# Kernel tuning notes

Measured on AMD Instinct MI355X. Metric: run time of the kernel, lower is better.

The kernel has to match this reference:

```python
import jax, jax.numpy as jnp
import numpy as np

I, H = 1, 16  # input_size, hidden_size


def setup_inputs() -> dict:
    key = jax.random.key(0)
    ks = jax.random.split(key, 7)
    B, T = 8192, 512
    s_ih = 1.0 / np.sqrt(H)
    return {
        "x": jax.random.normal(ks[0], (B, T, I), dtype=jnp.float32),
        "W_ih": jax.random.uniform(ks[1], (3 * H, I), minval=-s_ih, maxval=s_ih, dtype=jnp.float32),
        "W_hh": jax.random.uniform(ks[2], (3 * H, H), minval=-s_ih, maxval=s_ih, dtype=jnp.float32),
        "b_ih": jax.random.uniform(ks[3], (3 * H,), minval=-s_ih, maxval=s_ih, dtype=jnp.float32),
        "b_hh": jax.random.uniform(ks[4], (3 * H,), minval=-s_ih, maxval=s_ih, dtype=jnp.float32),
        "fc_w": jax.random.uniform(ks[5], (1, H), minval=-s_ih, maxval=s_ih, dtype=jnp.float32),
        "fc_b": jax.random.uniform(ks[6], (1,), minval=-s_ih, maxval=s_ih, dtype=jnp.float32),
    }


def _gru_last_hidden(x, W_ih, W_hh, b_ih, b_hh):
    # Precompute input projections for all timesteps: [B, T, 3H]
    xp = jnp.einsum("bti,gi->btg", x, W_ih) + b_ih
    xp = jnp.transpose(xp, (1, 0, 2))  # [T, B, 3H] for scan over time
    B = x.shape[0]
    h0 = jnp.zeros((B, H), dtype=x.dtype)

    def step(h, xt):
        # PyTorch GRU gate equations (gate order: r, z, n)
        gh = h @ W_hh.T + b_hh  # [B, 3H]
        xr, xz, xn = xt[:, :H], xt[:, H:2 * H], xt[:, 2 * H:]
        hr, hz, hn = gh[:, :H], gh[:, H:2 * H], gh[:, 2 * H:]
        r = jax.nn.sigmoid(xr + hr)
        z = jax.nn.sigmoid(xz + hz)
        n = jnp.tanh(xn + r * hn)
        h_new = (1.0 - z) * n + z * h
        return h_new, None

    h_last, _ = jax.lax.scan(step, h0, xp)
    return h_last  # [B, H]


def reference(x, W_ih, W_hh, b_ih, b_hh, fc_w, fc_b):
    # Dropout is identity in eval mode
    h_last = _gru_last_hidden(x, W_ih, W_hh, b_ih, b_hh)
    return h_last @ fc_w.T + fc_b  # [B, 1]
```

## Files before the change

### kernel.cpp

```cpp
#include <hip/hip_runtime.h>

namespace {

constexpr int T_LEN = 512;
constexpr float LOG2E = 1.4426950408889634f;

typedef _Float16 half4 __attribute__((ext_vector_type(4)));
typedef _Float16 half2v __attribute__((ext_vector_type(2)));
typedef float v4f __attribute__((ext_vector_type(4)));

__device__ __forceinline__ float fexp2(float a) {
#if __has_builtin(__builtin_amdgcn_exp2f)
    return __builtin_amdgcn_exp2f(a);
#else
    return exp2f(a);
#endif
}

__device__ __forceinline__ v4f mfma16h(half4 a, half4 b, v4f c) {
#if __has_builtin(__builtin_amdgcn_mfma_f32_16x16x16f16)
    return __builtin_amdgcn_mfma_f32_16x16x16f16(a, b, c, 0, 0, 0);
#else
    v4f d;
    asm volatile("v_mfma_f32_16x16x16_f16 %0, %1, %2, %3\n\ts_nop 7\n\ts_nop 7"
                 : "=v"(d) : "v"(a), "v"(b), "v"(c));
    return d;
#endif
}

__device__ __forceinline__ unsigned pk_f16(float a, float b) {
#if __has_builtin(__builtin_amdgcn_cvt_pkrtz)
    return __builtin_bit_cast(unsigned, __builtin_amdgcn_cvt_pkrtz(a, b));
#else
    half2v r; r[0] = (_Float16)a; r[1] = (_Float16)b;
    return __builtin_bit_cast(unsigned, r);
#endif
}

template<int OFF>
__device__ __forceinline__ unsigned ds_swz_u(unsigned v) {
    return (unsigned)__builtin_amdgcn_ds_swizzle((int)v, OFF);
}

__device__ __forceinline__ float gru_pair(float drp, float dzp, float dnp,
                                          float xt, float wihn, float bihn,
                                          float hp) {
    float Er = fexp2(drp);
    float Ez = fexp2(dzp);
    float pr = 1.0f + Er;
    float pz = 1.0f + Ez;
    float ip = __builtin_amdgcn_rcpf(pr * pz);
    float r  = ip * pz;
    float z  = ip * pr;
    float xn = __builtin_fmaf(xt, wihn, bihn);
    float v  = __builtin_fmaf(r, dnp, xn);
    float n  = __builtin_fmaf(-2.0f, __builtin_amdgcn_rcpf(1.0f + fexp2(v)), 1.0f);
    return __builtin_fmaf(z, hp - n, n);
}

__global__ __launch_bounds__(64) void gru_mfma8(
        const float* __restrict__ x,
        const float* __restrict__ W_ih,
        const float* __restrict__ W_hh,
        const float* __restrict__ b_ih,
        const float* __restrict__ b_hh,
        const float* __restrict__ fc_w,
        const float* __restrict__ fc_b,
        float* __restrict__ out) {
    const int L  = threadIdx.x;
    const int e  = L & 15;
    const int g  = L >> 4;
    const int jD = g * 4;
    const int ehi  = (e >> 3) & 1;
    const int ecol = e & 7;
    const int be   = blockIdx.x * 8 + ecol;
    const int r0   = jD + 2 * ehi;

    const float sR = -LOG2E;
    const float sN = 2.0f * LOG2E;

    half4 ar_hi, ar_lo, az_hi, az_lo, an_hi, an_lo;
#pragma unroll
    for (int i = 0; i < 4; ++i) {
        float wr = W_hh[(0  + e) * 16 + jD + i] * sR;
        float wz = W_hh[(16 + e) * 16 + jD + i] * sR;
        float wn = W_hh[(32 + e) * 16 + jD + i] * sN;
        _Float16 rh = (_Float16)wr; ar_hi[i] = rh; ar_lo[i] = (_Float16)(wr - (float)rh);
        _Float16 zh = (_Float16)wz; az_hi[i] = zh; az_lo[i] = (_Float16)(wz - (float)zh);
        _Float16 nh = (_Float16)wn; an_hi[i] = nh; an_lo[i] = (_Float16)(wn - (float)nh);
    }

    float wihr[4], wihz[4], biasr[4], biasz[4];
    v4f cn_const;
#pragma unroll
    for (int i = 0; i < 4; ++i) {
        int rj = jD + i;
        wihr[i]  = W_ih[rj]      * sR;
        wihz[i]  = W_ih[16 + rj] * sR;
        biasr[i] = (b_ih[rj]      + b_hh[rj])      * sR;
        biasz[i] = (b_ih[16 + rj] + b_hh[16 + rj]) * sR;
        cn_const[i] = b_hh[32 + rj] * sN;
    }
    const float wihn0 = W_ih[32 + r0]     * sN;
    const float wihn1 = W_ih[32 + r0 + 1] * sN;
    const float bihn0 = b_ih[32 + r0]     * sN;
    const float bihn1 = b_ih[32 + r0 + 1] * sN;

    const float4* xb = (const float4*)(x + (size_t)be * T_LEN);
    float4 xc0 = xb[0], xc1 = xb[1], xc2 = xb[2], xc3 = xb[3];

    float hp0 = 0.f, hp1 = 0.f;
    uint2 hz; hz.x = 0u; hz.y = 0u;
    half4 hf = __builtin_bit_cast(half4, hz);

#pragma unroll 1
    for (int c = 0; c < T_LEN / 16; ++c) {
        float4 xn0, xn1, xn2, xn3;
        if (c + 1 < T_LEN / 16) {
            xn0 = xb[(c + 1) * 4 + 0];
            xn1 = xb[(c + 1) * 4 + 1];
            xn2 = xb[(c + 1) * 4 + 2];
            xn3 = xb[(c + 1) * 4 + 3];
        }
#pragma unroll
        for (int s = 0; s < 16; ++s) {
            float4 q4 = (s < 4) ? xc0 : (s < 8) ? xc1 : (s < 12) ? xc2 : xc3;
            float xt  = ((s & 3) == 0) ? q4.x : ((s & 3) == 1) ? q4.y
                      : ((s & 3) == 2) ? q4.z : q4.w;

            v4f cr, cz;
#pragma unroll
            for (int i = 0; i < 4; ++i) {
                cr[i] = __builtin_fmaf(xt, wihr[i], biasr[i]);
                cz[i] = __builtin_fmaf(xt, wihz[i], biasz[i]);
            }
            v4f dr = mfma16h(ar_hi, hf, cr);
            v4f dz = mfma16h(az_hi, hf, cz);
            v4f dn = mfma16h(an_hi, hf, cn_const);
            dr = mfma16h(ar_lo, hf, dr);
            dz = mfma16h(az_lo, hf, dz);
            dn = mfma16h(an_lo, hf, dn);

            float d_r0 = ehi ? dr[2] : dr[0];
            float d_r1 = ehi ? dr[3] : dr[1];
            float d_z0 = ehi ? dz[2] : dz[0];
            float d_z1 = ehi ? dz[3] : dz[1];
            float d_n0 = ehi ? dn[2] : dn[0];
            float d_n1 = ehi ? dn[3] : dn[1];

            float h0n = gru_pair(d_r0, d_z0, d_n0, xt, wihn0, bihn0, hp0);
            float h1n = gru_pair(d_r1, d_z1, d_n1, xt, wihn1, bihn1, hp1);
            hp0 = h0n; hp1 = h1n;

            unsigned mine = pk_f16(h0n, h1n);
            unsigned oth  = ds_swz_u<0x201F>(mine);
            uint2 hv;
            hv.x = ehi ? oth  : mine;
            hv.y = ehi ? mine : oth;
            hf = __builtin_bit_cast(half4, hv);
        }
        if (c + 1 < T_LEN / 16) { xc0 = xn0; xc1 = xn1; xc2 = xn2; xc3 = xn3; }
    }

    float p = hp0 * fc_w[r0] + hp1 * fc_w[r0 + 1];
    p += __shfl_xor(p, 8, 64);
    p += __shfl_xor(p, 16, 64);
    p += __shfl_xor(p, 32, 64);
    if (L < 8) out[blockIdx.x * 8 + L] = p + fc_b[0];
}

}

extern "C" void kernel_launch(void* const* d_in, const int* in_sizes, int n_in,
                              void* d_out, int out_size, void* d_ws, size_t ws_size,
                              hipStream_t stream) {
    const float* x    = (const float*)d_in[0];
    const float* W_ih = (const float*)d_in[1];
    const float* W_hh = (const float*)d_in[2];
    const float* b_ih = (const float*)d_in[3];
    const float* b_hh = (const float*)d_in[4];
    const float* fc_w = (const float*)d_in[5];
    const float* fc_b = (const float*)d_in[6];
    float* out = (float*)d_out;

    const int B = out_size;
    const int blocks = B / 8;
    gru_mfma8<<<blocks, 64, 0, stream>>>(x, W_ih, W_hh, b_ih, b_hh,
                                         fc_w, fc_b, out);
}
```

Before: 107.2 us.

## Map four batch columns per wave so each lane computes one hidden unit

Each 64-lane wave now handles 4 batch elements instead of 8, so every lane owns a single hidden unit rather than two. This halves the per-lane transcendental and gate arithmetic on the serial critical path and doubles the number of blocks. The cost is an extra swizzle per step to gather the hidden state for the MFMA operand, the same six MFMAs per step covering half as many batch items, and twice the total MFMA work.

```diff
diff --git a/kernel.cpp b/kernel.cpp
--- a/kernel.cpp
+++ b/kernel.cpp
@@ -42,6 +42,12 @@
     return (unsigned)__builtin_amdgcn_ds_swizzle((int)v, OFF);
 }
 
+__device__ __forceinline__ float sel4(v4f d, bool qb0, bool qb1) {
+    float a = qb0 ? d[1] : d[0];
+    float b = qb0 ? d[3] : d[2];
+    return qb1 ? b : a;
+}
+
 __device__ __forceinline__ float gru_pair(float drp, float dzp, float dnp,
                                           float xt, float wihn, float bihn,
                                           float hp) {
@@ -58,7 +64,7 @@
     return __builtin_fmaf(z, hp - n, n);
 }
 
-__global__ __launch_bounds__(64) void gru_mfma8(
+__global__ __launch_bounds__(64) void gru_mfma4(
         const float* __restrict__ x,
         const float* __restrict__ W_ih,
         const float* __restrict__ W_hh,
@@ -71,10 +77,12 @@
     const int e  = L & 15;
     const int g  = L >> 4;
     const int jD = g * 4;
-    const int ehi  = (e >> 3) & 1;
-    const int ecol = e & 7;
-    const int be   = blockIdx.x * 8 + ecol;
-    const int r0   = jD + 2 * ehi;
+    const int q    = (e >> 2) & 3;
+    const bool qb0 = (q & 1) != 0;
+    const bool qb1 = (q & 2) != 0;
+    const int ecol = e & 3;
+    const int be   = blockIdx.x * 4 + ecol;
+    const int rme  = jD + q;
 
     const float sR = -LOG2E;
     const float sN = 2.0f * LOG2E;
@@ -101,15 +109,13 @@
         biasz[i] = (b_ih[16 + rj] + b_hh[16 + rj]) * sR;
         cn_const[i] = b_hh[32 + rj] * sN;
     }
-    const float wihn0 = W_ih[32 + r0]     * sN;
-    const float wihn1 = W_ih[32 + r0 + 1] * sN;
-    const float bihn0 = b_ih[32 + r0]     * sN;
-    const float bihn1 = b_ih[32 + r0 + 1] * sN;
+    const float wihn_ = W_ih[32 + rme] * sN;
+    const float bihn_ = b_ih[32 + rme] * sN;
 
     const float4* xb = (const float4*)(x + (size_t)be * T_LEN);
     float4 xc0 = xb[0], xc1 = xb[1], xc2 = xb[2], xc3 = xb[3];
 
-    float hp0 = 0.f, hp1 = 0.f;
+    float hp = 0.f;
     uint2 hz; hz.x = 0u; hz.y = 0u;
     half4 hf = __builtin_bit_cast(half4, hz);
 
@@ -141,32 +147,33 @@
             dz = mfma16h(az_lo, hf, dz);
             dn = mfma16h(an_lo, hf, dn);
 
-            float d_r0 = ehi ? dr[2] : dr[0];
-            float d_r1 = ehi ? dr[3] : dr[1];
-            float d_z0 = ehi ? dz[2] : dz[0];
-            float d_z1 = ehi ? dz[3] : dz[1];
-            float d_n0 = ehi ? dn[2] : dn[0];
-            float d_n1 = ehi ? dn[3] : dn[1];
+            float d_r = sel4(dr, qb0, qb1);
+            float d_z = sel4(dz, qb0, qb1);
+            float d_n = sel4(dn, qb0, qb1);
+            float hn = gru_pair(d_r, d_z, d_n, xt, wihn_, bihn_, hp);
+            hp = hn;
 
-            float h0n = gru_pair(d_r0, d_z0, d_n0, xt, wihn0, bihn0, hp0);
-            float h1n = gru_pair(d_r1, d_z1, d_n1, xt, wihn1, bihn1, hp1);
-            hp0 = h0n; hp1 = h1n;
-
-            unsigned mine = pk_f16(h0n, h1n);
-            unsigned oth  = ds_swz_u<0x201F>(mine);
+            unsigned hbits = __builtin_bit_cast(unsigned, hn);
+            unsigned p4    = ds_swz_u<0x101F>(hbits);
+            float hprt = __builtin_bit_cast(float, p4);
+            float plo = qb0 ? hprt : hn;
+            float phi = qb0 ? hn   : hprt;
+            unsigned pairu = pk_f16(plo, phi);
+            unsigned oth   = ds_swz_u<0x201F>(pairu);
             uint2 hv;
-            hv.x = ehi ? oth  : mine;
-            hv.y = ehi ? mine : oth;
+            hv.x = qb1 ? oth   : pairu;
+            hv.y = qb1 ? pairu : oth;
             hf = __builtin_bit_cast(half4, hv);
         }
         if (c + 1 < T_LEN / 16) { xc0 = xn0; xc1 = xn1; xc2 = xn2; xc3 = xn3; }
     }
 
-    float p = hp0 * fc_w[r0] + hp1 * fc_w[r0 + 1];
+    float p = hp * fc_w[rme];
+    p += __shfl_xor(p, 4, 64);
     p += __shfl_xor(p, 8, 64);
     p += __shfl_xor(p, 16, 64);
     p += __shfl_xor(p, 32, 64);
-    if (L < 8) out[blockIdx.x * 8 + L] = p + fc_b[0];
+    if (L < 4) out[blockIdx.x * 4 + L] = p + fc_b[0];
 }
 
 }
@@ -184,7 +191,7 @@
     float* out = (float*)d_out;
 
     const int B = out_size;
-    const int blocks = B / 8;
-    gru_mfma8<<<blocks, 64, 0, stream>>>(x, W_ih, W_hh, b_ih, b_hh,
+    const int blocks = B / 4;
+    gru_mfma4<<<blocks, 64, 0, stream>>>(x, W_ih, W_hh, b_ih, b_hh,
                                          fc_w, fc_b, out);
 }
```

Result: slower. 154.6 us (+44.2%).
